# Performance work log

Hardware: AMD Instinct MI355X
Metric: run time of the kernel (lower is better)

The kernel has to match this reference:

```python
import jax, jax.numpy as jnp
import numpy as np

EPS = 1e-9          # numerator epsilon from the original code
COS_EPS = 1e-8      # torch cosine_similarity clamps norms at 1e-8


def setup_inputs() -> dict:
    key = jax.random.key(0)
    kx, ky = jax.random.split(key)
    N, D = 8192, 1024
    x = jax.random.normal(kx, (N, D), dtype=jnp.float32)
    y = jax.random.randint(ky, (N,), 0, 10, dtype=jnp.int64)
    T = jnp.ones((1,), dtype=jnp.float32)
    return {"x": x, "y": y, "T": T}


def reference(x, y, T):
    # Soft Nearest Neighbor Loss with cosine distance, vectorized.
    # fits(i, j) = exp(-(1 - cos_sim(x_i, x_j)) / T)
    N = x.shape[0]
    norms = jnp.maximum(jnp.linalg.norm(x, axis=1, keepdims=True), COS_EPS)
    xn = x / norms                                   # [N, D] unit vectors
    sim = xn @ xn.T                                  # [N, N] cosine similarity
    f = jnp.exp(-(1.0 - sim) / T[0])                 # [N, N] fits

    off_diag = ~jnp.eye(N, dtype=bool)               # exclude i == j
    same = (y[:, None] == y[None, :]) & off_diag     # same-label pairs

    top = jnp.sum(jnp.where(same, f, 0.0), axis=1)   # [N]
    bot = jnp.sum(jnp.where(off_diag, f, 0.0), axis=1)
    loss = -jnp.mean(jnp.log((top + EPS) / bot))
    return loss
```

## Files before the change

kernel.cpp:

```cpp
#include <hip/hip_runtime.h>

#define NROWS 8192
#define DDIM  1024

typedef short  bf16x8 __attribute__((ext_vector_type(8)));
typedef float  f32x4  __attribute__((ext_vector_type(4)));
typedef unsigned short ushort_t;

__device__ __forceinline__ ushort_t f2bf(float f) {
    union { float f; unsigned u; } v; v.f = f;
    unsigned r = v.u + 0x7fffu + ((v.u >> 16) & 1u);
    return (ushort_t)(r >> 16);
}

#define GLD(gp, lp)                                                        \
    __builtin_amdgcn_global_load_lds(                                      \
        (const __attribute__((address_space(1))) void*)(gp),               \
        (__attribute__((address_space(3))) void*)(lp), 16, 0, 0)

__global__ __launch_bounds__(256) void snnl_normalize(
    const float* __restrict__ x, ushort_t* __restrict__ xn,
    float* __restrict__ top, float* __restrict__ bot, float* __restrict__ out)
{
    const int tid  = (int)threadIdx.x;
    const int lane = tid & 63;
    const int row  = (int)blockIdx.x * 4 + (tid >> 6);
    if (lane == 0) { top[row] = 0.0f; bot[row] = 0.0f; }
    if (row == 0 && lane == 0) out[0] = 0.0f;

    const float4* xr = (const float4*)(x + (size_t)row * DDIM);
    float4 v[4];
#pragma unroll
    for (int st = 0; st < 4; ++st) v[st] = xr[st * 64 + lane];
    float ss = 0.0f;
#pragma unroll
    for (int st = 0; st < 4; ++st)
        ss += v[st].x * v[st].x + v[st].y * v[st].y
            + v[st].z * v[st].z + v[st].w * v[st].w;
#pragma unroll
    for (int m = 32; m >= 1; m >>= 1) ss += __shfl_xor(ss, m);
    const float inv = 1.0f / fmaxf(sqrtf(ss), 1e-8f);
    ushort4* xo = (ushort4*)(xn + (size_t)row * DDIM);
#pragma unroll
    for (int st = 0; st < 4; ++st) {
        ushort4 o;
        o.x = f2bf(v[st].x * inv);
        o.y = f2bf(v[st].y * inv);
        o.z = f2bf(v[st].z * inv);
        o.w = f2bf(v[st].w * inv);
        xo[st * 64 + lane] = o;
    }
}

__global__ __launch_bounds__(256, 2) void snnl_main(
    const ushort_t* __restrict__ xn, const int* __restrict__ y,
    const float* __restrict__ T,
    float* __restrict__ top, float* __restrict__ bot)
{
    const int bid = (int)blockIdx.x;
    int rem = (bid & 7) * 260 + (bid >> 3);
    int p = 0, q = 0;
    {
        bool done = false;
        for (int qq = 0; qq < 8 && !done; ++qq) {
            for (int pp = 0; pp <= qq; ++pp) {
                const int c = (pp == qq) ? 36 : 64;
                if (rem < c) { p = pp; q = qq; done = true; break; }
                rem -= c;
            }
        }
    }
    int ti, tj;
    if (p == q) {
        int t = rem; tj = 7;
        for (int cc = 0; cc < 8; ++cc) {
            if (t <= cc) { tj = cc; break; }
            t -= (cc + 1);
        }
        ti = t;
    } else {
        ti = rem & 7; tj = rem >> 3;
    }
    const int bi = p * 8 + ti;
    const int bj = q * 8 + tj;
    const bool strict = (bi < bj);

    __shared__ char smem[57344];
    __shared__ int  yrow_s[128];
    __shared__ int  ycol_s[128];

    const int tid  = (int)threadIdx.x;
    const int lane = tid & 63;
    const int w    = tid >> 6;
    const int wr   = w >> 1;
    const int wc   = w & 1;
    const int i0   = bi * 128;
    const int j0   = bj * 128;

    if (tid < 128) yrow_s[tid] = y[i0 + tid];
    else           ycol_s[tid - 128] = y[j0 + tid - 128];

    const float invT = 1.0f / T[0];

    const int  rr  = tid >> 3;
    const int  scb = (((tid & 7) ^ (rr & 7)) << 4);
    const char* const xb = (const char*)xn;

    const int c0 = (((lane >> 4) << 4)) ^ ((lane & 7) << 4);
    int arow[4], brow[4];
#pragma unroll
    for (int mi = 0; mi < 4; ++mi) arow[mi] = (wr * 64 + mi * 16 + (lane & 15)) * 128;
#pragma unroll
    for (int ni = 0; ni < 4; ++ni) brow[ni] = 16384 + (wc * 64 + ni * 16 + (lane & 15)) * 128;

    const f32x4 zero4 = {0.0f, 0.0f, 0.0f, 0.0f};
    f32x4 acc[4][4];
#pragma unroll
    for (int mi = 0; mi < 4; ++mi)
#pragma unroll
        for (int ni = 0; ni < 4; ++ni) acc[mi][ni] = zero4;

    for (int kt = 0; kt < 16; ++kt) {
        const size_t kb = ((size_t)kt << 7) + (size_t)scb;
#pragma unroll
        for (int qq = 0; qq < 4; ++qq)
            GLD(xb + (((size_t)(i0 + qq * 32 + rr)) << 11) + kb,
                smem + (qq << 12) + (tid << 4));
#pragma unroll
        for (int qq = 0; qq < 4; ++qq)
            GLD(xb + (((size_t)(j0 + qq * 32 + rr)) << 11) + kb,
                smem + 16384 + (qq << 12) + (tid << 4));
        __syncthreads();

#pragma unroll
        for (int ks = 0; ks < 2; ++ks) {
            const int cks = c0 ^ (ks << 6);
            bf16x8 af[4], bfr[4];
#pragma unroll
            for (int mi = 0; mi < 4; ++mi)
                af[mi] = *(const bf16x8*)(smem + arow[mi] + cks);
#pragma unroll
            for (int ni = 0; ni < 4; ++ni)
                bfr[ni] = *(const bf16x8*)(smem + brow[ni] + cks);
#pragma unroll
            for (int mi = 0; mi < 4; ++mi)
#pragma unroll
                for (int ni = 0; ni < 4; ++ni)
                    acc[mi][ni] = __builtin_amdgcn_mfma_f32_16x16x32_bf16(
                        af[mi], bfr[ni], acc[mi][ni], 0, 0, 0);
        }
        __syncthreads();
    }

    int yjv[4], jgv[4];
#pragma unroll
    for (int ni = 0; ni < 4; ++ni) {
        const int jloc = wc * 64 + ni * 16 + (lane & 15);
        yjv[ni] = ycol_s[jloc];
        jgv[ni] = j0 + jloc;
    }
    float ct[4], cb[4];
#pragma unroll
    for (int ni = 0; ni < 4; ++ni) { ct[ni] = 0.0f; cb[ni] = 0.0f; }

#pragma unroll
    for (int mi = 0; mi < 4; ++mi) {
#pragma unroll
        for (int r = 0; r < 4; ++r) {
            const int il = wr * 64 + mi * 16 + ((lane >> 4) << 2) + r;
            const int ig = i0 + il;
            const int yi = yrow_s[il];
            float ba = 0.0f, ta = 0.0f;
#pragma unroll
            for (int ni = 0; ni < 4; ++ni) {
                const float fv = __expf((acc[mi][ni][r] - 1.0f) * invT);
                const bool  sm = (yi == yjv[ni]);
                const float bv = (ig != jgv[ni]) ? fv : 0.0f;
                const float tv = sm ? bv : 0.0f;
                ba += bv;  ta += tv;
                cb[ni] += bv;  ct[ni] += tv;
            }
            ta += __shfl_xor(ta, 1); ta += __shfl_xor(ta, 2);
            ta += __shfl_xor(ta, 4); ta += __shfl_xor(ta, 8);
            ba += __shfl_xor(ba, 1); ba += __shfl_xor(ba, 2);
            ba += __shfl_xor(ba, 4); ba += __shfl_xor(ba, 8);
            if ((lane & 15) == 0) {
                atomicAdd(&top[ig], ta);
                atomicAdd(&bot[ig], ba);
            }
        }
    }

    if (strict) {
#pragma unroll
        for (int ni = 0; ni < 4; ++ni) {
            float tv = ct[ni], bv = cb[ni];
            tv += __shfl_xor(tv, 16); tv += __shfl_xor(tv, 32);
            bv += __shfl_xor(bv, 16); bv += __shfl_xor(bv, 32);
            if (lane < 16) {
                atomicAdd(&top[jgv[ni]], tv);
                atomicAdd(&bot[jgv[ni]], bv);
            }
        }
    }
}

__global__ __launch_bounds__(256) void snnl_loss(
    const float* __restrict__ top, const float* __restrict__ bot,
    float* __restrict__ out)
{
    const int tid = (int)threadIdx.x;
    const int i   = (int)blockIdx.x * 256 + tid;
    float s = __logf((top[i] + 1e-9f) / bot[i]);
#pragma unroll
    for (int m = 32; m >= 1; m >>= 1) s += __shfl_xor(s, m);
    __shared__ float w4[4];
    if ((tid & 63) == 0) w4[tid >> 6] = s;
    __syncthreads();
    if (tid == 0)
        atomicAdd(out, -(w4[0] + w4[1] + w4[2] + w4[3]) * (1.0f / (float)NROWS));
}

extern "C" void kernel_launch(void* const* d_in, const int* in_sizes, int n_in,
                              void* d_out, int out_size, void* d_ws, size_t ws_size,
                              hipStream_t stream)
{
    const float* x = (const float*)d_in[0];
    const int*   y = (const int*)d_in[1];
    const float* T = (const float*)d_in[2];
    float* out = (float*)d_out;

    char* ws = (char*)d_ws;
    ushort_t* xn  = (ushort_t*)ws;
    float*    top = (float*)(ws + (size_t)16 * 1024 * 1024);
    float*    bot = top + NROWS;

    snnl_normalize<<<NROWS / 4, 256, 0, stream>>>(x, xn, top, bot, out);
    snnl_main<<<2080, 256, 0, stream>>>(xn, y, T, top, bot);
    snnl_loss<<<NROWS / 256, 256, 0, stream>>>(top, bot, out);
}
```

Measured before the change: 189.6 us.

## Double-buffer LDS tiles to overlap global loads with MFMA compute

Adds a second 32KB LDS buffer and prefetches the next K-tile with global_load_lds while the current tile is read into registers and fed to MFMAs. The loop drops from two barriers to one per iteration, and load latency should be hidden behind compute. LDS grows to 64KB per block, which may cut occupancy from the 2 blocks per CU requested. Holding fragments for both k-substeps also raises register pressure.

```diff
diff --git a/kernel.cpp b/kernel.cpp
--- a/kernel.cpp
+++ b/kernel.cpp
@@ -85,7 +85,7 @@
     const int bj = q * 8 + tj;
     const bool strict = (bi < bj);
 
-    __shared__ char smem[57344];
+    __shared__ char smem[65536];
     __shared__ int  yrow_s[128];
     __shared__ int  ycol_s[128];
 
@@ -106,6 +106,20 @@
     const int  scb = (((tid & 7) ^ (rr & 7)) << 4);
     const char* const xb = (const char*)xn;
 
+#define STAGE(buf, kt)                                                     \
+    {                                                                      \
+        const size_t kb_ = ((size_t)(kt) << 7) + (size_t)scb;              \
+        char* sb_ = smem + ((buf) << 15);                                  \
+        _Pragma("unroll")                                                  \
+        for (int qq = 0; qq < 4; ++qq)                                     \
+            GLD(xb + (((size_t)(i0 + qq * 32 + rr)) << 11) + kb_,          \
+                sb_ + (qq << 12) + (tid << 4));                            \
+        _Pragma("unroll")                                                  \
+        for (int qq = 0; qq < 4; ++qq)                                     \
+            GLD(xb + (((size_t)(j0 + qq * 32 + rr)) << 11) + kb_,          \
+                sb_ + 16384 + (qq << 12) + (tid << 4));                    \
+    }
+
     const int c0 = (((lane >> 4) << 4)) ^ ((lane & 7) << 4);
     int arow[4], brow[4];
 #pragma unroll
@@ -120,36 +134,34 @@
 #pragma unroll
         for (int ni = 0; ni < 4; ++ni) acc[mi][ni] = zero4;
 
+    STAGE(0, 0);
+    __syncthreads();
+
+    int cur = 0;
     for (int kt = 0; kt < 16; ++kt) {
-        const size_t kb = ((size_t)kt << 7) + (size_t)scb;
-#pragma unroll
-        for (int qq = 0; qq < 4; ++qq)
-            GLD(xb + (((size_t)(i0 + qq * 32 + rr)) << 11) + kb,
-                smem + (qq << 12) + (tid << 4));
-#pragma unroll
-        for (int qq = 0; qq < 4; ++qq)
-            GLD(xb + (((size_t)(j0 + qq * 32 + rr)) << 11) + kb,
-                smem + 16384 + (qq << 12) + (tid << 4));
-        __syncthreads();
-
+        const int sb = cur << 15;
+        bf16x8 af[2][4], bfr[2][4];
 #pragma unroll
         for (int ks = 0; ks < 2; ++ks) {
             const int cks = c0 ^ (ks << 6);
-            bf16x8 af[4], bfr[4];
 #pragma unroll
             for (int mi = 0; mi < 4; ++mi)
-                af[mi] = *(const bf16x8*)(smem + arow[mi] + cks);
+                af[ks][mi] = *(const bf16x8*)(smem + sb + arow[mi] + cks);
 #pragma unroll
             for (int ni = 0; ni < 4; ++ni)
-                bfr[ni] = *(const bf16x8*)(smem + brow[ni] + cks);
+                bfr[ks][ni] = *(const bf16x8*)(smem + sb + brow[ni] + cks);
+        }
+        if (kt < 15) STAGE(cur ^ 1, kt + 1);
+#pragma unroll
+        for (int ks = 0; ks < 2; ++ks)
 #pragma unroll
             for (int mi = 0; mi < 4; ++mi)
 #pragma unroll
                 for (int ni = 0; ni < 4; ++ni)
                     acc[mi][ni] = __builtin_amdgcn_mfma_f32_16x16x32_bf16(
-                        af[mi], bfr[ni], acc[mi][ni], 0, 0, 0);
-        }
+                        af[ks][mi], bfr[ks][ni], acc[mi][ni], 0, 0, 0);
         __syncthreads();
+        cur ^= 1;
     }
 
     int yjv[4], jgv[4];
@@ -203,6 +215,7 @@
             }
         }
     }
+#undef STAGE
 }
 
 __global__ __launch_bounds__(256) void snnl_loss(
```

Measured after the change: 189.0 us. Within noise of the previous version (-0.3%).
